# Optimization experiments

Hardware: AMD Instinct MI355X
Metric: run time of the kernel (lower is better)

Reference implementation:

```python
import jax, jax.numpy as jnp
import numpy as np

# Model constants (match init_kwargs)
H = 256          # hidden_dim
NH = 4           # num_heads
L = 4            # gnn_layers
T = 4            # transformer_layers
KMAX = 10        # k_max for overlap embedding
MAXD = 32        # MAX_DIST
INC = 119        # in_channels (atom vocab)
ED = 5           # edge_dim (bond vocab)
B = 64           # graphs per batch
M_SUB = 32       # subgraphs per graph (m)
KNODE = 32       # nodes per subgraph (k)
S = B * M_SUB    # total subgraphs = 2048
N = S * KNODE    # flattened nodes = 65536
E = 131072       # intra-subgraph directed edges


def _ln(x, g, b):
    mu = x.mean(-1, keepdims=True)
    var = ((x - mu) ** 2).mean(-1, keepdims=True)
    return (x - mu) * jax.lax.rsqrt(var + 1e-5) * g + b


def setup_inputs() -> dict:
    key = jax.random.key(0)
    ks = iter(jax.random.split(key, 24))
    nk = lambda: next(ks)
    rn = lambda k_, shp: 0.02 * jax.random.normal(k_, shp, dtype=jnp.float32)

    x_ids = jax.random.randint(nk(), (N,), 0, INC)
    edge_ids = jax.random.randint(nk(), (E,), 0, ED)
    # intra-subgraph edges: endpoints stay within each block of KNODE nodes
    eps_per = E // S
    base = jnp.repeat(jnp.arange(S) * KNODE, eps_per)
    src = base + jax.random.randint(nk(), (E,), 0, KNODE)
    dst = base + jax.random.randint(nk(), (E,), 0, KNODE)
    ns = jax.random.randint(nk(), (S, KNODE), 0, 500)
    padm = jax.random.uniform(nk(), (S, KNODE)) < 0.1
    nodes_sampled = jnp.where(padm, -1, ns)
    dist = jax.random.randint(nk(), (N,), 0, MAXD + 1)
    lp = -5.0 * jax.random.uniform(nk(), (S,))

    return {
        'x_ids': x_ids, 'edge_ids': edge_ids, 'src': src, 'dst': dst,
        'nodes_sampled': nodes_sampled, 'dist': dist, 'lp': lp,
        'atom_emb': rn(nk(), (INC, H)), 'bond_emb': rn(nk(), (ED, H)),
        'dist_emb': rn(nk(), (MAXD + 1, H)),
        'logp_W': rn(nk(), (H,)), 'logp_b': jnp.zeros((H,)),
        'gnn_eps': jnp.zeros((L,)),
        'gnn_W1': rn(nk(), (L, H, H)), 'gnn_b1': jnp.zeros((L, H)),
        'gnn_W2': rn(nk(), (L, H, H)), 'gnn_b2': jnp.zeros((L, H)),
        'ln1_g': jnp.ones((T, H)), 'ln1_b': jnp.zeros((T, H)),
        'qkv_W': rn(nk(), (T, H, 3 * H)),
        'out_W': rn(nk(), (T, H, H)), 'out_b': jnp.zeros((T, H)),
        'ln2_g': jnp.ones((T, H)), 'ln2_b': jnp.zeros((T, H)),
        'f1_W': rn(nk(), (T, H, 4 * H)), 'f1_b': jnp.zeros((T, 4 * H)),
        'f2_W': rn(nk(), (T, 4 * H, H)), 'f2_b': jnp.zeros((T, H)),
        'lnout_g': jnp.ones((H,)), 'lnout_b': jnp.zeros((H,)),
        'overlap_emb': rn(nk(), (KMAX + 1,)),
        'ht_alpha': jnp.ones(()),
    }


def reference(x_ids, edge_ids, src, dst, nodes_sampled, dist, lp,
              atom_emb, bond_emb, dist_emb, logp_W, logp_b,
              gnn_eps, gnn_W1, gnn_b1, gnn_W2, gnn_b2,
              ln1_g, ln1_b, qkv_W, out_W, out_b, ln2_g, ln2_b,
              f1_W, f1_b, f2_W, f2_b, lnout_g, lnout_b,
              overlap_emb, ht_alpha):
    # ---- flatten / embed node features ----
    valid = (nodes_sampled >= 0).reshape(N)
    valid_f = valid.astype(jnp.float32)[:, None]
    lp = jnp.where(jnp.isfinite(lp), lp, 0.0)
    sub_batch = jnp.arange(N) // KNODE
    dist_c = jnp.clip(dist, 0, MAXD)
    logp_pe = jax.nn.relu(lp[sub_batch][:, None] * logp_W + logp_b)
    h = (atom_emb[x_ids] + dist_emb[dist_c] + logp_pe) * valid_f  # [N,H]
    e = bond_emb[edge_ids]                                        # [E,H]

    # ---- GINE message passing ----
    for l in range(L):
        msg = jax.nn.relu(h[src] + e)                       # [E,H] gather
        agg = jax.ops.segment_sum(msg, dst, num_segments=N) # [N,H] scatter-add
        z = (1.0 + gnn_eps[l]) * h + agg
        z = jax.nn.relu(z @ gnn_W1[l] + gnn_b1[l])
        h = (z @ gnn_W2[l] + gnn_b2[l]) * valid_f

    # ---- pool roots into [B, m, H] tokens ----
    root = jnp.arange(S) * KNODE
    x = h[root].reshape(B, M_SUB, H)
    lp2 = lp.reshape(B, M_SUB)

    # ---- pairwise subgraph overlap bias ----
    nodes = nodes_sampled.reshape(B, M_SUB, KNODE)
    vmask = nodes >= 0
    # eq[b,i,j,ki,kj]: node ki of subgraph i equals node kj of subgraph j
    eq = nodes[:, :, None, :, None] == nodes[:, None, :, None, :]
    overlap = (eq.any(-1) & vmask[:, :, None, :]).sum(-1)  # [B,m,m]
    lp_c = jnp.clip(lp2, -30.0, 0.0)
    bias = overlap_emb[jnp.clip(overlap, 0, KMAX)] - ht_alpha * lp_c[:, None, :]
    bias = bias[:, None]  # [B,1,m,m], broadcast over heads

    # ---- relative-bias transformer ----
    hd = H // NH
    scale = 1.0 / np.sqrt(hd).astype(np.float32)
    for t in range(T):
        r = _ln(x, ln1_g[t], ln1_b[t])
        q, k_, v = jnp.split(r @ qkv_W[t], 3, axis=-1)
        q = q.reshape(B, M_SUB, NH, hd)
        k_ = k_.reshape(B, M_SUB, NH, hd)
        v = v.reshape(B, M_SUB, NH, hd)
        scores = jnp.einsum('bihd,bjhd->bhij', q, k_) * scale + bias
        attn = jax.nn.softmax(scores, axis=-1)
        o = jnp.einsum('bhij,bjhd->bihd', attn, v).reshape(B, M_SUB, H)
        x = x + o @ out_W[t] + out_b[t]
        r2 = _ln(x, ln2_g[t], ln2_b[t])
        x = x + jax.nn.gelu(r2 @ f1_W[t] + f1_b[t], approximate=False) @ f2_W[t] + f2_b[t]

    x = _ln(x, lnout_g, lnout_b)
    # HT-weighted mean over subgraph tokens
    w = jax.nn.softmax(-lp_c, axis=1)
    return (w[:, :, None] * x).sum(1)  # [B,H]
```

## Files before the change

### kernel.cpp

```cpp
#include <hip/hip_runtime.h>
#include <hip/hip_bf16.h>
#include <math.h>

#define HDIM   256
#define NHEAD  4
#define LLAY   4
#define TLAY   4
#define KMAXC  10
#define MAXD   32
#define BATCH  64
#define MSUB   32
#define KNODE  32
#define SSUB   2048
#define NNODE  65536
#define NEDGE  131072
#define EPSPER 64
#define EDN    5

typedef unsigned short u16;
typedef __attribute__((ext_vector_type(8))) short bf16x8;
typedef __attribute__((ext_vector_type(4))) float f32x4;

__device__ __forceinline__ float us2f(u16 u) {
    union { unsigned int i; float f; } x; x.i = ((unsigned int)u) << 16; return x.f;
}
__device__ __forceinline__ u16 f2us(float v) {
    union { float f; unsigned int i; } x; x.f = v;
    unsigned int u = x.i;
    u += 0x7fffu + ((u >> 16) & 1u);
    return (u16)(u >> 16);
}
__device__ __forceinline__ float finite_or_zero(float v) {
    return (v == v && fabsf(v) <= 3.0e38f) ? v : 0.0f;
}
__device__ __forceinline__ void gll16(const u16* g, u16* l) {
    __builtin_amdgcn_global_load_lds(
        (const __attribute__((address_space(1))) unsigned int*)g,
        (__attribute__((address_space(3))) unsigned int*)l, 16, 0, 0);
}

__global__ __launch_bounds__(256) void k_csr(
    const int* __restrict__ src, const int* __restrict__ dst,
    const int* __restrict__ eid, u16* __restrict__ perm, u16* __restrict__ off)
{
    __shared__ int sL[4][64], dL[4][64], eL[4][64];
    int wave = threadIdx.x >> 6, lane = threadIdx.x & 63;
    int sgi = blockIdx.x * 4 + wave;
    sL[wave][lane] = src[sgi * 64 + lane] - sgi * KNODE;
    dL[wave][lane] = dst[sgi * 64 + lane] - sgi * KNODE;
    eL[wave][lane] = eid[sgi * 64 + lane];
    __syncthreads();
    if (lane < 32) {
        int cnt = 0;
        for (int e = 0; e < 64; ++e) cnt += (dL[wave][e] == lane) ? 1 : 0;
        int incl = cnt;
        #pragma unroll
        for (int d = 1; d < 32; d <<= 1) {
            int v = __shfl_up(incl, d, 64);
            if (lane >= d) incl += v;
        }
        int start = incl - cnt;
        off[sgi * 32 + lane] = (u16)start;
        int pos = start;
        for (int e = 0; e < 64; ++e) {
            if (dL[wave][e] == lane) {
                perm[sgi * 64 + pos] = (u16)((sL[wave][e] << 3) | eL[wave][e]);
                ++pos;
            }
        }
    }
}

__global__ __launch_bounds__(256) void k_wtrans(
    const float* __restrict__ W, u16* __restrict__ WT, int K, int N)
{
    __shared__ float til[32][33];
    int k0 = blockIdx.x * 32, n0 = blockIdx.y * 32, s = blockIdx.z;
    const float* Wb = W + (size_t)s * K * N;
    u16* Tb = WT + (size_t)s * N * K;
    int j = threadIdx.x & 31, i0 = threadIdx.x >> 5;
    #pragma unroll
    for (int it = 0; it < 4; ++it) {
        int i = i0 + it * 8;
        til[i][j] = Wb[(size_t)(k0 + i) * N + n0 + j];
    }
    __syncthreads();
    #pragma unroll
    for (int it = 0; it < 4; ++it) {
        int i = i0 + it * 8;
        Tb[(size_t)(n0 + i) * K + k0 + j] = f2us(til[j][i]);
    }
}

__global__ __launch_bounds__(256, 4) void k_gnn4(
    const int* __restrict__ x_ids, const int* __restrict__ dist,
    const int* __restrict__ nodes, const float* __restrict__ lp,
    const float* __restrict__ atom_emb, const float* __restrict__ dist_emb,
    const float* __restrict__ logp_W, const float* __restrict__ logp_b,
    const u16* __restrict__ perm, const u16* __restrict__ off,
    const float* __restrict__ bond_emb, const float* __restrict__ eps_arr,
    const float* __restrict__ b1a, const float* __restrict__ b2a,
    const u16* __restrict__ W1T, const u16* __restrict__ W2T,
    float* __restrict__ x)
{
    __shared__ __align__(16) unsigned char smem[38912];
    u16*   hz    = (u16*)smem;
    float* bondL = (float*)(smem + 32768);
    u16*   permL = (u16*)(smem + 32768 + 5120);
    u16*   offL  = (u16*)(smem + 32768 + 5120 + 256);
    float* validL= (float*)(smem + 32768 + 5120 + 512);
    float* epsL  = (float*)(smem + 32768 + 5120 + 512 + 256);

    int tid = threadIdx.x, lane = tid & 63, wave = tid >> 6;
    int row0 = blockIdx.x * 64;
    int fr = lane & 15, quad = lane >> 4;

    for (int i = tid; i < EDN * 256; i += 256) bondL[i] = bond_emb[i];
    if (tid < 128) permL[tid] = perm[blockIdx.x * 128 + tid];
    if (tid < 64) {
        offL[tid] = off[blockIdx.x * 64 + tid];
        validL[tid] = (nodes[row0 + tid] >= 0) ? 1.0f : 0.0f;
    }
    if (tid < 4) epsL[tid] = eps_arr[tid];

    {
        int m = tid & 63, qd = tid >> 6;
        int rg = row0 + m;
        float valid = (nodes[rg] >= 0) ? 1.0f : 0.0f;
        float lpv = finite_or_zero(lp[rg >> 5]);
        int dc = dist[rg]; dc = dc < 0 ? 0 : (dc > MAXD ? MAXD : dc);
        int xid = x_ids[rg];
        #pragma unroll
        for (int k = 0; k < 8; ++k) {
            int cc = qd * 8 + k, c = cc * 8;
            float4 a0 = *reinterpret_cast<const float4*>(atom_emb + xid * 256 + c);
            float4 a1 = *reinterpret_cast<const float4*>(atom_emb + xid * 256 + c + 4);
            float4 d0 = *reinterpret_cast<const float4*>(dist_emb + dc * 256 + c);
            float4 d1 = *reinterpret_cast<const float4*>(dist_emb + dc * 256 + c + 4);
            float4 w0 = *reinterpret_cast<const float4*>(logp_W + c);
            float4 w1 = *reinterpret_cast<const float4*>(logp_W + c + 4);
            float4 p0 = *reinterpret_cast<const float4*>(logp_b + c);
            float4 p1 = *reinterpret_cast<const float4*>(logp_b + c + 4);
            union { bf16x8 v; ushort4 h[2]; } o;
            o.h[0] = (ushort4){
                f2us((a0.x + d0.x + fmaxf(lpv * w0.x + p0.x, 0.f)) * valid),
                f2us((a0.y + d0.y + fmaxf(lpv * w0.y + p0.y, 0.f)) * valid),
                f2us((a0.z + d0.z + fmaxf(lpv * w0.z + p0.z, 0.f)) * valid),
                f2us((a0.w + d0.w + fmaxf(lpv * w0.w + p0.w, 0.f)) * valid) };
            o.h[1] = (ushort4){
                f2us((a1.x + d1.x + fmaxf(lpv * w1.x + p1.x, 0.f)) * valid),
                f2us((a1.y + d1.y + fmaxf(lpv * w1.y + p1.y, 0.f)) * valid),
                f2us((a1.z + d1.z + fmaxf(lpv * w1.z + p1.z, 0.f)) * valid),
                f2us((a1.w + d1.w + fmaxf(lpv * w1.w + p1.w, 0.f)) * valid) };
            *reinterpret_cast<bf16x8*>(hz + m * 256 + ((cc ^ (m & 7)) * 8)) = o.v;
        }
    }
    __syncthreads();

    int rl = tid >> 3, g8 = tid & 7;
    for (int l = 0; l < LLAY; ++l) {
        float ep1 = 1.0f + epsL[l];
        for (int p = 0; p < 2; ++p) {
            int row = p * 32 + rl;
            int e0 = offL[p * 32 + rl];
            int e1 = (rl < 31) ? offL[p * 32 + rl + 1] : 64;
            float a[32];
            #pragma unroll
            for (int q = 0; q < 32; ++q) a[q] = 0.f;
            for (int j = e0; j < e1; ++j) {
                int ent = permL[p * 64 + j];
                int sl = p * 32 + (ent >> 3);
                int be = ent & 7;
                #pragma unroll
                for (int q = 0; q < 4; ++q) {
                    union { bf16x8 v; u16 s[8]; } hv;
                    hv.v = *reinterpret_cast<const bf16x8*>(
                        hz + sl * 256 + (((g8 * 4 + q) ^ (sl & 7)) * 8));
                    const float* bp = bondL + be * 256 + g8 * 32 + q * 8;
                    float4 bo0 = *reinterpret_cast<const float4*>(bp);
                    float4 bo1 = *reinterpret_cast<const float4*>(bp + 4);
                    a[q*8+0] += fmaxf(us2f(hv.s[0]) + bo0.x, 0.f);
                    a[q*8+1] += fmaxf(us2f(hv.s[1]) + bo0.y, 0.f);
                    a[q*8+2] += fmaxf(us2f(hv.s[2]) + bo0.z, 0.f);
                    a[q*8+3] += fmaxf(us2f(hv.s[3]) + bo0.w, 0.f);
                    a[q*8+4] += fmaxf(us2f(hv.s[4]) + bo1.x, 0.f);
                    a[q*8+5] += fmaxf(us2f(hv.s[5]) + bo1.y, 0.f);
                    a[q*8+6] += fmaxf(us2f(hv.s[6]) + bo1.z, 0.f);
                    a[q*8+7] += fmaxf(us2f(hv.s[7]) + bo1.w, 0.f);
                }
            }
            __syncthreads();
            #pragma unroll
            for (int q = 0; q < 4; ++q) {
                u16* ptr = hz + row * 256 + (((g8 * 4 + q) ^ (row & 7)) * 8);
                union { bf16x8 v; u16 s[8]; } hv, ov;
                hv.v = *reinterpret_cast<const bf16x8*>(ptr);
                #pragma unroll
                for (int k = 0; k < 8; ++k)
                    ov.s[k] = f2us(ep1 * us2f(hv.s[k]) + a[q * 8 + k]);
                *reinterpret_cast<bf16x8*>(ptr) = ov.v;
            }
        }
        __syncthreads();

        const u16* W1 = W1T + l * 65536;
        const float* b1 = b1a + l * 256;
        bf16x8 wf[4][8];
        #pragma unroll
        for (int i = 0; i < 4; ++i)
            #pragma unroll
            for (int kc = 0; kc < 8; ++kc)
                wf[i][kc] = *reinterpret_cast<const bf16x8*>(
                    W1 + (size_t)(wave * 64 + i * 16 + fr) * 256 + kc * 32 + quad * 8);
        f32x4 acc[4][4];
        #pragma unroll
        for (int i = 0; i < 4; ++i)
            #pragma unroll
            for (int j = 0; j < 4; ++j) acc[i][j] = (f32x4){0.f, 0.f, 0.f, 0.f};
        #pragma unroll
        for (int kc = 0; kc < 8; ++kc) {
            bf16x8 bfv[4];
            #pragma unroll
            for (int j = 0; j < 4; ++j) {
                int m = j * 16 + fr;
                bfv[j] = *reinterpret_cast<const bf16x8*>(hz + m * 256 + (((kc * 4 + quad) ^ (m & 7)) * 8));
            }
            #pragma unroll
            for (int i = 0; i < 4; ++i)
                #pragma unroll
                for (int j = 0; j < 4; ++j)
                    acc[i][j] = __builtin_amdgcn_mfma_f32_16x16x32_bf16(wf[i][kc], bfv[j], acc[i][j], 0, 0, 0);
        }
        __syncthreads();
        #pragma unroll
        for (int i = 0; i < 4; ++i) {
            int n1b = wave * 64 + i * 16 + quad * 4;
            float4 bb = *reinterpret_cast<const float4*>(b1 + n1b);
            #pragma unroll
            for (int j = 0; j < 4; ++j) {
                int m = j * 16 + fr;
                ushort4 o = { f2us(fmaxf(acc[i][j][0] + bb.x, 0.f)),
                              f2us(fmaxf(acc[i][j][1] + bb.y, 0.f)),
                              f2us(fmaxf(acc[i][j][2] + bb.z, 0.f)),
                              f2us(fmaxf(acc[i][j][3] + bb.w, 0.f)) };
                *reinterpret_cast<ushort4*>(hz + m * 256 + (((n1b >> 3) ^ (m & 7)) * 8) + (n1b & 7)) = o;
            }
        }
        __syncthreads();

        const u16* W2 = W2T + l * 65536;
        const float* b2 = b2a + l * 256;
        #pragma unroll
        for (int i = 0; i < 4; ++i)
            #pragma unroll
            for (int kc = 0; kc < 8; ++kc)
                wf[i][kc] = *reinterpret_cast<const bf16x8*>(
                    W2 + (size_t)(wave * 64 + i * 16 + fr) * 256 + kc * 32 + quad * 8);
        #pragma unroll
        for (int i = 0; i < 4; ++i)
            #pragma unroll
            for (int j = 0; j < 4; ++j) acc[i][j] = (f32x4){0.f, 0.f, 0.f, 0.f};
        #pragma unroll
        for (int kc = 0; kc < 8; ++kc) {
            bf16x8 bfv[4];
            #pragma unroll
            for (int j = 0; j < 4; ++j) {
                int m = j * 16 + fr;
                bfv[j] = *reinterpret_cast<const bf16x8*>(hz + m * 256 + (((kc * 4 + quad) ^ (m & 7)) * 8));
            }
            #pragma unroll
            for (int i = 0; i < 4; ++i)
                #pragma unroll
                for (int j = 0; j < 4; ++j)
                    acc[i][j] = __builtin_amdgcn_mfma_f32_16x16x32_bf16(wf[i][kc], bfv[j], acc[i][j], 0, 0, 0);
        }
        __syncthreads();

        if (l < LLAY - 1) {
            #pragma unroll
            for (int i = 0; i < 4; ++i) {
                int n2b = wave * 64 + i * 16 + quad * 4;
                float4 bb = *reinterpret_cast<const float4*>(b2 + n2b);
                #pragma unroll
                for (int j = 0; j < 4; ++j) {
                    int m = j * 16 + fr;
                    float vm = validL[m];
                    ushort4 o = { f2us((acc[i][j][0] + bb.x) * vm),
                                  f2us((acc[i][j][1] + bb.y) * vm),
                                  f2us((acc[i][j][2] + bb.z) * vm),
                                  f2us((acc[i][j][3] + bb.w) * vm) };
                    *reinterpret_cast<ushort4*>(hz + m * 256 + (((n2b >> 3) ^ (m & 7)) * 8) + (n2b & 7)) = o;
                }
            }
            __syncthreads();
        } else {
            if (fr == 0) {
                #pragma unroll
                for (int i = 0; i < 4; ++i) {
                    int n2b = wave * 64 + i * 16 + quad * 4;
                    float4 bb = *reinterpret_cast<const float4*>(b2 + n2b);
                    #pragma unroll
                    for (int jj = 0; jj < 2; ++jj) {
                        int j = jj * 2, m = j * 16;
                        float vm = validL[m];
                        float4 o = { (acc[i][j][0] + bb.x) * vm,
                                     (acc[i][j][1] + bb.y) * vm,
                                     (acc[i][j][2] + bb.z) * vm,
                                     (acc[i][j][3] + bb.w) * vm };
                        *reinterpret_cast<float4*>(
                            x + (size_t)(blockIdx.x * 2 + (m >> 5)) * 256 + n2b) = o;
                    }
                }
            }
        }
    }
}

__global__ __launch_bounds__(256) void k_tgemm64(
    const u16* __restrict__ A, const u16* __restrict__ BT,
    const float* __restrict__ bias, void* __restrict__ Cout, int c_is_bf16,
    const float* __restrict__ resid, const int* __restrict__ valid,
    int M, int K, int N, int act)
{
    __shared__ __align__(16) u16 As[2][64 * 32];
    __shared__ __align__(16) u16 Bs[2][64 * 32];
    int tid = threadIdx.x, lane = tid & 63, wave = tid >> 6;
    int wm = wave >> 1, wn = wave & 1;
    int bm = blockIdx.y * 64, bn = blockIdx.x * 64;
    const u16* gA = A + (size_t)(bm + wave * 16 + (lane >> 2)) * K + (lane & 3) * 8;
    const u16* gB = BT + (size_t)(bn + wave * 16 + (lane >> 2)) * K + (lane & 3) * 8;
    gll16(gA, &As[0][wave * 512]);
    gll16(gB, &Bs[0][wave * 512]);
    f32x4 acc[2][2];
    #pragma unroll
    for (int i = 0; i < 2; ++i)
        #pragma unroll
        for (int j = 0; j < 2; ++j) acc[i][j] = (f32x4){0.f, 0.f, 0.f, 0.f};
    int fr = lane & 15, quad = lane >> 4;
    int nit = K >> 5;
    __syncthreads();
    for (int it = 0; it < nit; ++it) {
        int buf = it & 1;
        if (it + 1 < nit) {
            int k0 = (it + 1) * 32;
            gll16(gA + k0, &As[buf ^ 1][wave * 512]);
            gll16(gB + k0, &Bs[buf ^ 1][wave * 512]);
        }
        bf16x8 af[2], bfr[2];
        #pragma unroll
        for (int i = 0; i < 2; ++i)
            af[i] = *reinterpret_cast<const bf16x8*>(&As[buf][(wm * 32 + i * 16 + fr) * 32 + quad * 8]);
        #pragma unroll
        for (int j = 0; j < 2; ++j)
            bfr[j] = *reinterpret_cast<const bf16x8*>(&Bs[buf][(wn * 32 + j * 16 + fr) * 32 + quad * 8]);
        #pragma unroll
        for (int i = 0; i < 2; ++i)
            #pragma unroll
            for (int j = 0; j < 2; ++j)
                acc[i][j] = __builtin_amdgcn_mfma_f32_16x16x32_bf16(af[i], bfr[j], acc[i][j], 0, 0, 0);
        __syncthreads();
    }
    int crow0 = bm + wm * 32 + quad * 4;
    int ccol0 = bn + wn * 32 + fr;
    #pragma unroll
    for (int i = 0; i < 2; ++i) {
        #pragma unroll
        for (int r = 0; r < 4; ++r) {
            int m = crow0 + i * 16 + r;
            float vm = valid ? ((valid[m] >= 0) ? 1.0f : 0.0f) : 1.0f;
            #pragma unroll
            for (int j = 0; j < 2; ++j) {
                int n = ccol0 + j * 16;
                float v = acc[i][j][r];
                if (bias) v += bias[n];
                if (act == 1) v = v > 0.f ? v : 0.f;
                else if (act == 2) v = 0.5f * v * (1.0f + erff(v * 0.70710678118654752f));
                v *= vm;
                if (resid) v += resid[(size_t)m * N + n];
                if (c_is_bf16) ((u16*)Cout)[(size_t)m * N + n] = f2us(v);
                else ((float*)Cout)[(size_t)m * N + n] = v;
            }
        }
    }
}

__global__ __launch_bounds__(256) void k_ln(
    const float* __restrict__ X, u16* __restrict__ Out,
    const float* __restrict__ g, const float* __restrict__ b)
{
    int row = blockIdx.x * 4 + (threadIdx.x >> 6);
    int lane = threadIdx.x & 63;
    float4 xv = *reinterpret_cast<const float4*>(X + (size_t)row * HDIM + lane * 4);
    float s = xv.x + xv.y + xv.z + xv.w;
    #pragma unroll
    for (int off = 32; off > 0; off >>= 1) s += __shfl_xor(s, off);
    float mu = s * (1.0f / HDIM);
    float d0 = xv.x - mu, d1 = xv.y - mu, d2 = xv.z - mu, d3 = xv.w - mu;
    float sq = d0 * d0 + d1 * d1 + d2 * d2 + d3 * d3;
    #pragma unroll
    for (int off = 32; off > 0; off >>= 1) sq += __shfl_xor(sq, off);
    float rs = rsqrtf(sq * (1.0f / HDIM) + 1e-5f);
    int c = lane * 4;
    float4 gv = *reinterpret_cast<const float4*>(g + c);
    float4 bv = *reinterpret_cast<const float4*>(b + c);
    ushort4 o = { f2us(d0 * rs * gv.x + bv.x), f2us(d1 * rs * gv.y + bv.y),
                  f2us(d2 * rs * gv.z + bv.z), f2us(d3 * rs * gv.w + bv.w) };
    *reinterpret_cast<ushort4*>(Out + (size_t)row * HDIM + c) = o;
}

__global__ __launch_bounds__(1024) void k_bias(
    const int* __restrict__ nodes, const float* __restrict__ lp,
    const float* __restrict__ ovl_emb, const float* __restrict__ alpha_p,
    float* __restrict__ bias)
{
    int b = blockIdx.x, tid = threadIdx.x;
    __shared__ int nd[32][32];
    __shared__ unsigned int bmv[32][17];
    __shared__ float lpc[32];
    __shared__ float emb[16];
    nd[tid >> 5][tid & 31] = nodes[b * 1024 + tid];
    if (tid < 512) bmv[tid >> 4][tid & 15] = 0u;
    if (tid < 32) {
        float l = finite_or_zero(lp[b * 32 + tid]);
        l = l < -30.f ? -30.f : (l > 0.f ? 0.f : l);
        lpc[tid] = l;
    }
    if (tid >= 64 && tid < 64 + KMAXC + 1) emb[tid - 64] = ovl_emb[tid - 64];
    __syncthreads();
    int own = nd[tid >> 5][tid & 31];
    if (own >= 0) atomicOr(&bmv[tid >> 5][own >> 5], 1u << (own & 31));
    __syncthreads();
    int i = tid >> 5, j = tid & 31;
    float alpha = alpha_p[0];
    int cnt = 0;
    #pragma unroll
    for (int k = 0; k < 32; ++k) {
        int nk = nd[i][k];
        if (nk >= 0) cnt += (int)((bmv[j][nk >> 5] >> (nk & 31)) & 1u);
    }
    bias[b * 1024 + tid] = emb[cnt > KMAXC ? KMAXC : cnt] - alpha * lpc[j];
}

__global__ __launch_bounds__(256) void k_attn(
    const u16* __restrict__ qkv, const float* __restrict__ bias, u16* __restrict__ o)
{
    int b = blockIdx.x >> 2, hh = blockIdx.x & 3;
    __shared__ float qs[32][65], ks[32][65], vs[32][65];
    __shared__ float sc[32][33];
    int tid = threadIdx.x;
    #pragma unroll
    for (int u = 0; u < 8; ++u) {
        int idx = tid + u * 256;
        int i = idx >> 6, d = idx & 63;
        size_t base = (size_t)(b * 32 + i) * 768;
        qs[i][d] = us2f(qkv[base + hh * 64 + d]);
        ks[i][d] = us2f(qkv[base + 256 + hh * 64 + d]);
        vs[i][d] = us2f(qkv[base + 512 + hh * 64 + d]);
    }
    __syncthreads();
    #pragma unroll
    for (int u = 0; u < 4; ++u) {
        int p = tid + u * 256;
        int i = p >> 5, j = p & 31;
        float s = 0.f;
        #pragma unroll
        for (int d = 0; d < 64; ++d) s += qs[i][d] * ks[j][d];
        sc[i][j] = s * 0.125f + bias[b * 1024 + i * 32 + j];
    }
    __syncthreads();
    if (tid < 32) {
        int i = tid;
        float m = -1e30f;
        for (int j = 0; j < 32; ++j) m = fmaxf(m, sc[i][j]);
        float sum = 0.f;
        for (int j = 0; j < 32; ++j) { float e = expf(sc[i][j] - m); sc[i][j] = e; sum += e; }
        float inv = 1.0f / sum;
        for (int j = 0; j < 32; ++j) sc[i][j] *= inv;
    }
    __syncthreads();
    #pragma unroll
    for (int u = 0; u < 8; ++u) {
        int idx = tid + u * 256;
        int i = idx >> 6, d = idx & 63;
        float a = 0.f;
        #pragma unroll
        for (int j = 0; j < 32; ++j) a += sc[i][j] * vs[j][d];
        o[(size_t)(b * 32 + i) * HDIM + hh * 64 + d] = f2us(a);
    }
}

__global__ __launch_bounds__(256) void k_final(
    const u16* __restrict__ xln, const float* __restrict__ lp, float* __restrict__ out)
{
    int b = blockIdx.x, tid = threadIdx.x;
    __shared__ float w[32];
    if (tid < 32) {
        float l = finite_or_zero(lp[b * 32 + tid]);
        l = l < -30.f ? -30.f : (l > 0.f ? 0.f : l);
        w[tid] = -l;
    }
    __syncthreads();
    if (tid == 0) {
        float m = -1e30f;
        for (int i = 0; i < 32; ++i) m = fmaxf(m, w[i]);
        float s = 0.f;
        for (int i = 0; i < 32; ++i) { float e = expf(w[i] - m); w[i] = e; s += e; }
        float inv = 1.0f / s;
        for (int i = 0; i < 32; ++i) w[i] *= inv;
    }
    __syncthreads();
    float acc = 0.f;
    for (int i = 0; i < 32; ++i) acc += w[i] * us2f(xln[(size_t)(b * 32 + i) * HDIM + tid]);
    out[b * HDIM + tid] = acc;
}

extern "C" void kernel_launch(void* const* d_in, const int* in_sizes, int n_in,
                              void* d_out, int out_size, void* d_ws, size_t ws_size,
                              hipStream_t stream)
{
    const int*   x_ids    = (const int*)d_in[0];
    const int*   edge_ids = (const int*)d_in[1];
    const int*   srcp     = (const int*)d_in[2];
    const int*   dstp     = (const int*)d_in[3];
    const int*   nodes    = (const int*)d_in[4];
    const int*   dist     = (const int*)d_in[5];
    const float* lp       = (const float*)d_in[6];
    const float* atom_emb = (const float*)d_in[7];
    const float* bond_emb = (const float*)d_in[8];
    const float* dist_emb = (const float*)d_in[9];
    const float* logp_W   = (const float*)d_in[10];
    const float* logp_b   = (const float*)d_in[11];
    const float* gnn_eps  = (const float*)d_in[12];
    const float* gnn_W1   = (const float*)d_in[13];
    const float* gnn_b1   = (const float*)d_in[14];
    const float* gnn_W2   = (const float*)d_in[15];
    const float* gnn_b2   = (const float*)d_in[16];
    const float* ln1_g    = (const float*)d_in[17];
    const float* ln1_b    = (const float*)d_in[18];
    const float* qkv_W    = (const float*)d_in[19];
    const float* out_W    = (const float*)d_in[20];
    const float* out_b    = (const float*)d_in[21];
    const float* ln2_g    = (const float*)d_in[22];
    const float* ln2_b    = (const float*)d_in[23];
    const float* f1_W     = (const float*)d_in[24];
    const float* f1_b     = (const float*)d_in[25];
    const float* f2_W     = (const float*)d_in[26];
    const float* f2_b     = (const float*)d_in[27];
    const float* lnout_g  = (const float*)d_in[28];
    const float* lnout_b  = (const float*)d_in[29];
    const float* ovl_emb  = (const float*)d_in[30];
    const float* alpha    = (const float*)d_in[31];

    char* ws = (char*)d_ws;
    u16*   gW1T  = (u16*)(ws + 100663296ull);
    u16*   gW2T  = (u16*)(ws + 100663296ull + 524288ull);
    u16*   permW = (u16*)(ws + 100663296ull + 1048576ull);
    u16*   offW  = (u16*)(ws + 100663296ull + 1310720ull);
    u16*   r     = (u16*)(ws + 33554432ull);
    u16*   ob    = (u16*)(ws + 33554432ull + 1048576ull);
    u16*   qkvb  = (u16*)(ws + 33554432ull + 2097152ull);
    u16*   ffh   = (u16*)(ws + 33554432ull + 5242880ull);
    u16*   xln   = (u16*)(ws + 33554432ull + 9437184ull);
    float* biasb = (float*)(ws + 33554432ull + 10485760ull);
    u16*   qkvT  = (u16*)(ws + 33554432ull + 11534336ull);
    u16*   outT  = (u16*)(ws + 33554432ull + 13107200ull);
    u16*   f1T   = (u16*)(ws + 33554432ull + 13631488ull);
    u16*   f2T   = (u16*)(ws + 33554432ull + 15728640ull);
    float* x     = (float*)(ws + 67108864ull);

    k_csr<<<SSUB / 4, 256, 0, stream>>>(srcp, dstp, edge_ids, permW, offW);
    k_wtrans<<<dim3(8, 8, 4), 256, 0, stream>>>(gnn_W1, gW1T, 256, 256);
    k_wtrans<<<dim3(8, 8, 4), 256, 0, stream>>>(gnn_W2, gW2T, 256, 256);
    k_gnn4<<<NNODE / 64, 256, 0, stream>>>(
        x_ids, dist, nodes, lp, atom_emb, dist_emb, logp_W, logp_b,
        permW, offW, bond_emb, gnn_eps, gnn_b1, gnn_b2, gW1T, gW2T, x);
    k_wtrans<<<dim3(8, 24, 4), 256, 0, stream>>>(qkv_W, qkvT, 256, 768);
    k_wtrans<<<dim3(8, 8, 4), 256, 0, stream>>>(out_W, outT, 256, 256);
    k_wtrans<<<dim3(8, 32, 4), 256, 0, stream>>>(f1_W, f1T, 256, 1024);
    k_wtrans<<<dim3(32, 8, 4), 256, 0, stream>>>(f2_W, f2T, 1024, 256);
    k_bias<<<BATCH, 1024, 0, stream>>>(nodes, lp, ovl_emb, alpha, biasb);
    for (int t = 0; t < TLAY; ++t) {
        k_ln<<<SSUB / 4, 256, 0, stream>>>(x, r, ln1_g + t * HDIM, ln1_b + t * HDIM);
        k_tgemm64<<<dim3(12, SSUB / 64), 256, 0, stream>>>(
            r, qkvT + t * 768 * 256, nullptr, qkvb, 1,
            nullptr, nullptr, SSUB, 256, 768, 0);
        k_attn<<<BATCH * NHEAD, 256, 0, stream>>>(qkvb, biasb, ob);
        k_tgemm64<<<dim3(4, SSUB / 64), 256, 0, stream>>>(
            ob, outT + t * 65536, out_b + t * HDIM, x, 0,
            x, nullptr, SSUB, 256, HDIM, 0);
        k_ln<<<SSUB / 4, 256, 0, stream>>>(x, r, ln2_g + t * HDIM, ln2_b + t * HDIM);
        k_tgemm64<<<dim3(16, SSUB / 64), 256, 0, stream>>>(
            r, f1T + t * 1024 * 256, f1_b + t * 1024, ffh, 1,
            nullptr, nullptr, SSUB, 256, 1024, 2);
        k_tgemm64<<<dim3(4, SSUB / 64), 256, 0, stream>>>(
            ffh, f2T + t * 256 * 1024, f2_b + t * HDIM, x, 0,
            x, nullptr, SSUB, 1024, HDIM, 0);
    }
    k_ln<<<SSUB / 4, 256, 0, stream>>>(x, xln, lnout_g, lnout_b);
    k_final<<<BATCH, 256, 0, stream>>>(xln, lp, (float*)d_out);
}
```

Measured before the change: 587.1 us.

## Fuse layernorm into transformer GEMM prologues and final pooling kernel

LayerNorm is now computed inside the QKV and FFN1 GEMM kernels: each block normalizes its 64 rows of the residual into a swizzled shared-memory A tile, removing the standalone LN kernels and their bf16 round trip through global memory. The final LN is merged with the weighted pooling kernel. The GNN kernel's launch bound drops from 4 to 3 blocks per SM, allowing more registers. The trade-off is that each column block recomputes the LN for its rows (12 or 16 times redundantly), and each block needs 32 KB of shared memory for the A tile.

```diff
diff --git a/kernel.cpp b/kernel.cpp
--- a/kernel.cpp
+++ b/kernel.cpp
@@ -92,7 +92,7 @@
     }
 }
 
-__global__ __launch_bounds__(256, 4) void k_gnn4(
+__global__ __launch_bounds__(256, 3) void k_gnn4(
     const int* __restrict__ x_ids, const int* __restrict__ dist,
     const int* __restrict__ nodes, const float* __restrict__ lp,
     const float* __restrict__ atom_emb, const float* __restrict__ dist_emb,
@@ -316,98 +316,6 @@
     }
 }
 
-__global__ __launch_bounds__(256) void k_tgemm64(
-    const u16* __restrict__ A, const u16* __restrict__ BT,
-    const float* __restrict__ bias, void* __restrict__ Cout, int c_is_bf16,
-    const float* __restrict__ resid, const int* __restrict__ valid,
-    int M, int K, int N, int act)
-{
-    __shared__ __align__(16) u16 As[2][64 * 32];
-    __shared__ __align__(16) u16 Bs[2][64 * 32];
-    int tid = threadIdx.x, lane = tid & 63, wave = tid >> 6;
-    int wm = wave >> 1, wn = wave & 1;
-    int bm = blockIdx.y * 64, bn = blockIdx.x * 64;
-    const u16* gA = A + (size_t)(bm + wave * 16 + (lane >> 2)) * K + (lane & 3) * 8;
-    const u16* gB = BT + (size_t)(bn + wave * 16 + (lane >> 2)) * K + (lane & 3) * 8;
-    gll16(gA, &As[0][wave * 512]);
-    gll16(gB, &Bs[0][wave * 512]);
-    f32x4 acc[2][2];
-    #pragma unroll
-    for (int i = 0; i < 2; ++i)
-        #pragma unroll
-        for (int j = 0; j < 2; ++j) acc[i][j] = (f32x4){0.f, 0.f, 0.f, 0.f};
-    int fr = lane & 15, quad = lane >> 4;
-    int nit = K >> 5;
-    __syncthreads();
-    for (int it = 0; it < nit; ++it) {
-        int buf = it & 1;
-        if (it + 1 < nit) {
-            int k0 = (it + 1) * 32;
-            gll16(gA + k0, &As[buf ^ 1][wave * 512]);
-            gll16(gB + k0, &Bs[buf ^ 1][wave * 512]);
-        }
-        bf16x8 af[2], bfr[2];
-        #pragma unroll
-        for (int i = 0; i < 2; ++i)
-            af[i] = *reinterpret_cast<const bf16x8*>(&As[buf][(wm * 32 + i * 16 + fr) * 32 + quad * 8]);
-        #pragma unroll
-        for (int j = 0; j < 2; ++j)
-            bfr[j] = *reinterpret_cast<const bf16x8*>(&Bs[buf][(wn * 32 + j * 16 + fr) * 32 + quad * 8]);
-        #pragma unroll
-        for (int i = 0; i < 2; ++i)
-            #pragma unroll
-            for (int j = 0; j < 2; ++j)
-                acc[i][j] = __builtin_amdgcn_mfma_f32_16x16x32_bf16(af[i], bfr[j], acc[i][j], 0, 0, 0);
-        __syncthreads();
-    }
-    int crow0 = bm + wm * 32 + quad * 4;
-    int ccol0 = bn + wn * 32 + fr;
-    #pragma unroll
-    for (int i = 0; i < 2; ++i) {
-        #pragma unroll
-        for (int r = 0; r < 4; ++r) {
-            int m = crow0 + i * 16 + r;
-            float vm = valid ? ((valid[m] >= 0) ? 1.0f : 0.0f) : 1.0f;
-            #pragma unroll
-            for (int j = 0; j < 2; ++j) {
-                int n = ccol0 + j * 16;
-                float v = acc[i][j][r];
-                if (bias) v += bias[n];
-                if (act == 1) v = v > 0.f ? v : 0.f;
-                else if (act == 2) v = 0.5f * v * (1.0f + erff(v * 0.70710678118654752f));
-                v *= vm;
-                if (resid) v += resid[(size_t)m * N + n];
-                if (c_is_bf16) ((u16*)Cout)[(size_t)m * N + n] = f2us(v);
-                else ((float*)Cout)[(size_t)m * N + n] = v;
-            }
-        }
-    }
-}
-
-__global__ __launch_bounds__(256) void k_ln(
-    const float* __restrict__ X, u16* __restrict__ Out,
-    const float* __restrict__ g, const float* __restrict__ b)
-{
-    int row = blockIdx.x * 4 + (threadIdx.x >> 6);
-    int lane = threadIdx.x & 63;
-    float4 xv = *reinterpret_cast<const float4*>(X + (size_t)row * HDIM + lane * 4);
-    float s = xv.x + xv.y + xv.z + xv.w;
-    #pragma unroll
-    for (int off = 32; off > 0; off >>= 1) s += __shfl_xor(s, off);
-    float mu = s * (1.0f / HDIM);
-    float d0 = xv.x - mu, d1 = xv.y - mu, d2 = xv.z - mu, d3 = xv.w - mu;
-    float sq = d0 * d0 + d1 * d1 + d2 * d2 + d3 * d3;
-    #pragma unroll
-    for (int off = 32; off > 0; off >>= 1) sq += __shfl_xor(sq, off);
-    float rs = rsqrtf(sq * (1.0f / HDIM) + 1e-5f);
-    int c = lane * 4;
-    float4 gv = *reinterpret_cast<const float4*>(g + c);
-    float4 bv = *reinterpret_cast<const float4*>(b + c);
-    ushort4 o = { f2us(d0 * rs * gv.x + bv.x), f2us(d1 * rs * gv.y + bv.y),
-                  f2us(d2 * rs * gv.z + bv.z), f2us(d3 * rs * gv.w + bv.w) };
-    *reinterpret_cast<ushort4*>(Out + (size_t)row * HDIM + c) = o;
-}
-
 __global__ __launch_bounds__(1024) void k_bias(
     const int* __restrict__ nodes, const float* __restrict__ lp,
     const float* __restrict__ ovl_emb, const float* __restrict__ alpha_p,
@@ -441,6 +349,155 @@
     bias[b * 1024 + tid] = emb[cnt > KMAXC ? KMAXC : cnt] - alpha * lpc[j];
 }
 
+__global__ __launch_bounds__(256) void k_gemmA_ln(
+    const float* __restrict__ X, const u16* __restrict__ BT,
+    const float* __restrict__ ln_g, const float* __restrict__ ln_b,
+    const float* __restrict__ bias, u16* __restrict__ C,
+    int N, int act)
+{
+    __shared__ __align__(16) u16 As[64 * 256];
+    __shared__ __align__(16) u16 Bs[2][64 * 32];
+    int tid = threadIdx.x, lane = tid & 63, wave = tid >> 6;
+    int wm = wave >> 1, wn = wave & 1;
+    int bm = blockIdx.y * 64, bn = blockIdx.x * 64;
+    int fr = lane & 15, quad = lane >> 4;
+
+    const u16* gB = BT + (size_t)(bn + wave * 16 + (lane >> 2)) * 256 + (lane & 3) * 8;
+    gll16(gB, &Bs[0][wave * 512]);
+
+    #pragma unroll
+    for (int rr = 0; rr < 16; ++rr) {
+        int r = wave * 16 + rr;
+        float4 xv = *reinterpret_cast<const float4*>(X + (size_t)(bm + r) * 256 + lane * 4);
+        float s = xv.x + xv.y + xv.z + xv.w;
+        #pragma unroll
+        for (int o2 = 32; o2 > 0; o2 >>= 1) s += __shfl_xor(s, o2);
+        float mu = s * (1.0f / 256.0f);
+        float d0 = xv.x - mu, d1 = xv.y - mu, d2 = xv.z - mu, d3 = xv.w - mu;
+        float sq = d0 * d0 + d1 * d1 + d2 * d2 + d3 * d3;
+        #pragma unroll
+        for (int o2 = 32; o2 > 0; o2 >>= 1) sq += __shfl_xor(sq, o2);
+        float rs = rsqrtf(sq * (1.0f / 256.0f) + 1e-5f);
+        int c = lane * 4;
+        float4 gv = *reinterpret_cast<const float4*>(ln_g + c);
+        float4 bv = *reinterpret_cast<const float4*>(ln_b + c);
+        ushort4 o = { f2us(d0 * rs * gv.x + bv.x), f2us(d1 * rs * gv.y + bv.y),
+                      f2us(d2 * rs * gv.z + bv.z), f2us(d3 * rs * gv.w + bv.w) };
+        *reinterpret_cast<ushort4*>(As + r * 256 + (((lane >> 1) ^ (r & 7)) * 8) + (lane & 1) * 4) = o;
+    }
+    __syncthreads();
+
+    f32x4 acc[2][2];
+    #pragma unroll
+    for (int i = 0; i < 2; ++i)
+        #pragma unroll
+        for (int j = 0; j < 2; ++j) acc[i][j] = (f32x4){0.f, 0.f, 0.f, 0.f};
+    for (int kc = 0; kc < 8; ++kc) {
+        int buf = kc & 1;
+        if (kc < 7) gll16(gB + (kc + 1) * 32, &Bs[buf ^ 1][wave * 512]);
+        bf16x8 af[2], bfr[2];
+        #pragma unroll
+        for (int i = 0; i < 2; ++i) {
+            int m = wm * 32 + i * 16 + fr;
+            af[i] = *reinterpret_cast<const bf16x8*>(As + m * 256 + (((kc * 4 + quad) ^ (m & 7)) * 8));
+        }
+        #pragma unroll
+        for (int j = 0; j < 2; ++j)
+            bfr[j] = *reinterpret_cast<const bf16x8*>(&Bs[buf][(wn * 32 + j * 16 + fr) * 32 + quad * 8]);
+        #pragma unroll
+        for (int i = 0; i < 2; ++i)
+            #pragma unroll
+            for (int j = 0; j < 2; ++j)
+                acc[i][j] = __builtin_amdgcn_mfma_f32_16x16x32_bf16(af[i], bfr[j], acc[i][j], 0, 0, 0);
+        __syncthreads();
+    }
+    int crow0 = bm + wm * 32 + quad * 4;
+    int ccol0 = bn + wn * 32 + fr;
+    #pragma unroll
+    for (int i = 0; i < 2; ++i) {
+        #pragma unroll
+        for (int r = 0; r < 4; ++r) {
+            int m = crow0 + i * 16 + r;
+            #pragma unroll
+            for (int j = 0; j < 2; ++j) {
+                int n = ccol0 + j * 16;
+                float v = acc[i][j][r];
+                if (bias) v += bias[n];
+                if (act == 2) v = 0.5f * v * (1.0f + erff(v * 0.70710678118654752f));
+                C[(size_t)m * N + n] = f2us(v);
+            }
+        }
+    }
+}
+
+__global__ __launch_bounds__(256) void k_gemmB(
+    const u16* __restrict__ A, const u16* __restrict__ BT,
+    const float* __restrict__ bias, void* __restrict__ Cout, int c_is_bf16,
+    const float* __restrict__ resid, const int* __restrict__ valid,
+    int M, int K, int N, int act)
+{
+    __shared__ __align__(16) u16 As[2][64 * 32];
+    __shared__ __align__(16) u16 Bs[2][64 * 32];
+    int tid = threadIdx.x, lane = tid & 63, wave = tid >> 6;
+    int wm = wave >> 1, wn = wave & 1;
+    int bm = blockIdx.y * 64, bn = blockIdx.x * 64;
+    const u16* gA = A + (size_t)(bm + wave * 16 + (lane >> 2)) * K + (lane & 3) * 8;
+    const u16* gB = BT + (size_t)(bn + wave * 16 + (lane >> 2)) * K + (lane & 3) * 8;
+    gll16(gA, &As[0][wave * 512]);
+    gll16(gB, &Bs[0][wave * 512]);
+    f32x4 acc[2][2];
+    #pragma unroll
+    for (int i = 0; i < 2; ++i)
+        #pragma unroll
+        for (int j = 0; j < 2; ++j) acc[i][j] = (f32x4){0.f, 0.f, 0.f, 0.f};
+    int fr = lane & 15, quad = lane >> 4;
+    int nit = K >> 5;
+    __syncthreads();
+    for (int it = 0; it < nit; ++it) {
+        int buf = it & 1;
+        if (it + 1 < nit) {
+            int k0 = (it + 1) * 32;
+            gll16(gA + k0, &As[buf ^ 1][wave * 512]);
+            gll16(gB + k0, &Bs[buf ^ 1][wave * 512]);
+        }
+        bf16x8 af[2], bfr[2];
+        #pragma unroll
+        for (int i = 0; i < 2; ++i)
+            af[i] = *reinterpret_cast<const bf16x8*>(&As[buf][(wm * 32 + i * 16 + fr) * 32 + quad * 8]);
+        #pragma unroll
+        for (int j = 0; j < 2; ++j)
+            bfr[j] = *reinterpret_cast<const bf16x8*>(&Bs[buf][(wn * 32 + j * 16 + fr) * 32 + quad * 8]);
+        #pragma unroll
+        for (int i = 0; i < 2; ++i)
+            #pragma unroll
+            for (int j = 0; j < 2; ++j)
+                acc[i][j] = __builtin_amdgcn_mfma_f32_16x16x32_bf16(af[i], bfr[j], acc[i][j], 0, 0, 0);
+        __syncthreads();
+    }
+    int crow0 = bm + wm * 32 + quad * 4;
+    int ccol0 = bn + wn * 32 + fr;
+    #pragma unroll
+    for (int i = 0; i < 2; ++i) {
+        #pragma unroll
+        for (int r = 0; r < 4; ++r) {
+            int m = crow0 + i * 16 + r;
+            float vm = valid ? ((valid[m] >= 0) ? 1.0f : 0.0f) : 1.0f;
+            #pragma unroll
+            for (int j = 0; j < 2; ++j) {
+                int n = ccol0 + j * 16;
+                float v = acc[i][j][r];
+                if (bias) v += bias[n];
+                if (act == 1) v = v > 0.f ? v : 0.f;
+                else if (act == 2) v = 0.5f * v * (1.0f + erff(v * 0.70710678118654752f));
+                v *= vm;
+                if (resid) v += resid[(size_t)m * N + n];
+                if (c_is_bf16) ((u16*)Cout)[(size_t)m * N + n] = f2us(v);
+                else ((float*)Cout)[(size_t)m * N + n] = v;
+            }
+        }
+    }
+}
+
 __global__ __launch_bounds__(256) void k_attn(
     const u16* __restrict__ qkv, const float* __restrict__ bias, u16* __restrict__ o)
 {
@@ -485,33 +542,58 @@
         float a = 0.f;
         #pragma unroll
         for (int j = 0; j < 32; ++j) a += sc[i][j] * vs[j][d];
-        o[(size_t)(b * 32 + i) * HDIM + hh * 64 + d] = f2us(a);
-    }
-}
-
-__global__ __launch_bounds__(256) void k_final(
-    const u16* __restrict__ xln, const float* __restrict__ lp, float* __restrict__ out)
-{
-    int b = blockIdx.x, tid = threadIdx.x;
-    __shared__ float w[32];
-    if (tid < 32) {
-        float l = finite_or_zero(lp[b * 32 + tid]);
-        l = l < -30.f ? -30.f : (l > 0.f ? 0.f : l);
-        w[tid] = -l;
+        o[(size_t)(b * 32 + i) * 256 + hh * 64 + d] = f2us(a);
+    }
+}
+
+__global__ __launch_bounds__(256) void k_fin(
+    const float* __restrict__ x, const float* __restrict__ lp,
+    const float* __restrict__ lnout_g, const float* __restrict__ lnout_b,
+    float* __restrict__ out)
+{
+    __shared__ __align__(16) float xlnf[32 * 260];
+    __shared__ float wfin[32];
+    int tid = threadIdx.x, lane = tid & 63, wave = tid >> 6;
+    int b = blockIdx.x;
+    #pragma unroll
+    for (int rr = 0; rr < 8; ++rr) {
+        int row = wave * 8 + rr;
+        float4 xv = *reinterpret_cast<const float4*>(x + (size_t)(b * 32 + row) * 256 + lane * 4);
+        float s = xv.x + xv.y + xv.z + xv.w;
+        #pragma unroll
+        for (int o2 = 32; o2 > 0; o2 >>= 1) s += __shfl_xor(s, o2);
+        float mu = s * (1.0f / 256.0f);
+        float d0 = xv.x - mu, d1 = xv.y - mu, d2 = xv.z - mu, d3 = xv.w - mu;
+        float sq = d0 * d0 + d1 * d1 + d2 * d2 + d3 * d3;
+        #pragma unroll
+        for (int o2 = 32; o2 > 0; o2 >>= 1) sq += __shfl_xor(sq, o2);
+        float rs = rsqrtf(sq * (1.0f / 256.0f) + 1e-5f);
+        int c = lane * 4;
+        float4 gv = *reinterpret_cast<const float4*>(lnout_g + c);
+        float4 bv = *reinterpret_cast<const float4*>(lnout_b + c);
+        float4 o = { d0 * rs * gv.x + bv.x, d1 * rs * gv.y + bv.y,
+                     d2 * rs * gv.z + bv.z, d3 * rs * gv.w + bv.w };
+        *reinterpret_cast<float4*>(xlnf + row * 260 + c) = o;
     }
     __syncthreads();
     if (tid == 0) {
+        float l2[32];
         float m = -1e30f;
-        for (int i = 0; i < 32; ++i) m = fmaxf(m, w[i]);
+        for (int i = 0; i < 32; ++i) {
+            float l = finite_or_zero(lp[b * 32 + i]);
+            l = l < -30.f ? -30.f : (l > 0.f ? 0.f : l);
+            l2[i] = -l;
+            m = fmaxf(m, -l);
+        }
         float s = 0.f;
-        for (int i = 0; i < 32; ++i) { float e = expf(w[i] - m); w[i] = e; s += e; }
+        for (int i = 0; i < 32; ++i) { float e = expf(l2[i] - m); wfin[i] = e; s += e; }
         float inv = 1.0f / s;
-        for (int i = 0; i < 32; ++i) w[i] *= inv;
-    }
-    __syncthreads();
-    float acc = 0.f;
-    for (int i = 0; i < 32; ++i) acc += w[i] * us2f(xln[(size_t)(b * 32 + i) * HDIM + tid]);
-    out[b * HDIM + tid] = acc;
+        for (int i = 0; i < 32; ++i) wfin[i] *= inv;
+    }
+    __syncthreads();
+    float a = 0.f;
+    for (int i = 0; i < 32; ++i) a += wfin[i] * xlnf[i * 260 + tid];
+    out[(size_t)b * 256 + tid] = a;
 }
 
 extern "C" void kernel_launch(void* const* d_in, const int* in_sizes, int n_in,
@@ -556,16 +638,14 @@
     u16*   gW2T  = (u16*)(ws + 100663296ull + 524288ull);
     u16*   permW = (u16*)(ws + 100663296ull + 1048576ull);
     u16*   offW  = (u16*)(ws + 100663296ull + 1310720ull);
-    u16*   r     = (u16*)(ws + 33554432ull);
-    u16*   ob    = (u16*)(ws + 33554432ull + 1048576ull);
-    u16*   qkvb  = (u16*)(ws + 33554432ull + 2097152ull);
-    u16*   ffh   = (u16*)(ws + 33554432ull + 5242880ull);
-    u16*   xln   = (u16*)(ws + 33554432ull + 9437184ull);
-    float* biasb = (float*)(ws + 33554432ull + 10485760ull);
-    u16*   qkvT  = (u16*)(ws + 33554432ull + 11534336ull);
-    u16*   outT  = (u16*)(ws + 33554432ull + 13107200ull);
-    u16*   f1T   = (u16*)(ws + 33554432ull + 13631488ull);
-    u16*   f2T   = (u16*)(ws + 33554432ull + 15728640ull);
+    u16*   qkvT  = (u16*)(ws + 33554432ull);
+    u16*   outT  = (u16*)(ws + 33554432ull + 1572864ull);
+    u16*   f1T   = (u16*)(ws + 33554432ull + 2097152ull);
+    u16*   f2T   = (u16*)(ws + 33554432ull + 4194304ull);
+    u16*   ob    = (u16*)(ws + 33554432ull + 6291456ull);
+    float* biasb = (float*)(ws + 33554432ull + 7340032ull);
+    u16*   qkvb  = (u16*)(ws + 33554432ull + 7602176ull);
+    u16*   ffh   = (u16*)(ws + 33554432ull + 10747904ull);
     float* x     = (float*)(ws + 67108864ull);
 
     k_csr<<<SSUB / 4, 256, 0, stream>>>(srcp, dstp, edge_ids, permW, offW);
@@ -580,22 +660,19 @@
     k_wtrans<<<dim3(32, 8, 4), 256, 0, stream>>>(f2_W, f2T, 1024, 256);
     k_bias<<<BATCH, 1024, 0, stream>>>(nodes, lp, ovl_emb, alpha, biasb);
     for (int t = 0; t < TLAY; ++t) {
-        k_ln<<<SSUB / 4, 256, 0, stream>>>(x, r, ln1_g + t * HDIM, ln1_b + t * HDIM);
-        k_tgemm64<<<dim3(12, SSUB / 64), 256, 0, stream>>>(
-            r, qkvT + t * 768 * 256, nullptr, qkvb, 1,
-            nullptr, nullptr, SSUB, 256, 768, 0);
+        k_gemmA_ln<<<dim3(12, 32), 256, 0, stream>>>(
+            x, qkvT + (size_t)t * 768 * 256, ln1_g + t * 256, ln1_b + t * 256,
+            nullptr, qkvb, 768, 0);
         k_attn<<<BATCH * NHEAD, 256, 0, stream>>>(qkvb, biasb, ob);
-        k_tgemm64<<<dim3(4, SSUB / 64), 256, 0, stream>>>(
-            ob, outT + t * 65536, out_b + t * HDIM, x, 0,
-            x, nullptr, SSUB, 256, HDIM, 0);
-        k_ln<<<SSUB / 4, 256, 0, stream>>>(x, r, ln2_g + t * HDIM, ln2_b + t * HDIM);
-        k_tgemm64<<<dim3(16, SSUB / 64), 256, 0, stream>>>(
-            r, f1T + t * 1024 * 256, f1_b + t * 1024, ffh, 1,
-            nullptr, nullptr, SSUB, 256, 1024, 2);
-        k_tgemm64<<<dim3(4, SSUB / 64), 256, 0, stream>>>(
-            ffh, f2T + t * 256 * 1024, f2_b + t * HDIM, x, 0,
-            x, nullptr, SSUB, 1024, HDIM, 0);
-    }
-    k_ln<<<SSUB / 4, 256, 0, stream>>>(x, xln, lnout_g, lnout_b);
-    k_final<<<BATCH, 256, 0, stream>>>(xln, lp, (float*)d_out);
-}
+        k_gemmB<<<dim3(4, 32), 256, 0, stream>>>(
+            ob, outT + (size_t)t * 65536, out_b + t * 256, x, 0,
+            x, nullptr, SSUB, 256, 256, 0);
+        k_gemmA_ln<<<dim3(16, 32), 256, 0, stream>>>(
+            x, f1T + (size_t)t * 1024 * 256, ln2_g + t * 256, ln2_b + t * 256,
+            f1_b + t * 1024, ffh, 1024, 2);
+        k_gemmB<<<dim3(4, 32), 256, 0, stream>>>(
+            ffh, f2T + (size_t)t * 256 * 1024, f2_b + t * 256, x, 0,
+            x, nullptr, SSUB, 1024, 256, 0);
+    }
+    k_fin<<<BATCH, 256, 0, stream>>>(x, lp, lnout_g, lnout_b, (float*)d_out);
+}
```

New measurement: 608.0 us. 1.04x slower.
